# Performance work log

Hardware: AMD Instinct MI355X
Metric: run time of the kernel (lower is better)

The kernel has to match this reference:

```python
import jax, jax.numpy as jnp
import numpy as np

B, S, R, H, NH, HD = 32, 1026, 256, 1024, 16, 64

def setup_inputs() -> dict:
    key = jax.random.key(0)
    ks = jax.random.split(key, 8)
    sc = 0.02
    return {
        "q_low": jax.random.normal(ks[0], (B, S, R), jnp.float32),
        "k_low": jax.random.normal(ks[1], (B, S, R), jnp.float32),
        "v_low": jax.random.normal(ks[2], (B, S, R), jnp.float32),
        "Wq": jax.random.normal(ks[3], (R, H), jnp.float32) * sc,
        "bq": jnp.zeros((H,), jnp.float32),
        "Wk": jax.random.normal(ks[4], (R, H), jnp.float32) * sc,
        "bk": jnp.zeros((H,), jnp.float32),
        "Wv": jax.random.normal(ks[5], (R, H), jnp.float32) * sc,
        "bv": jnp.zeros((H,), jnp.float32),
        "Wo_down": jax.random.normal(ks[6], (H, R), jnp.float32) * sc,
    }

def reference(q_low, k_low, v_low, Wq, bq, Wk, bk, Wv, bv, Wo_down):
    # Up-project low-rank activations to full Q, K, V: [B,S,R] @ [R,H] -> [B,S,H]
    q = q_low @ Wq + bq
    k = k_low @ Wk + bk
    v = v_low @ Wv + bv
    # split heads: [B,S,NH,HD] -> [B,NH,S,HD]
    def split(x):
        return x.reshape(B, S, NH, HD).transpose(0, 2, 1, 3)
    qh, kh, vh = split(q), split(k), split(v)
    scores = jnp.einsum('bhqd,bhkd->bhqk', qh, kh) / jnp.sqrt(jnp.float32(HD))
    probs = jax.nn.softmax(scores, axis=-1)  # dropout p=0
    ctx = jnp.einsum('bhqk,bhkd->bhqd', probs, vh)
    ctx = ctx.transpose(0, 2, 1, 3).reshape(B, S, H)
    # Down-project with low-rank activation (gelu)
    out_low = jax.nn.gelu(ctx @ Wo_down, approximate=False)
    return out_low
```

## Files before the change

### kernel.cpp

```cpp
#include <hip/hip_runtime.h>
#include <hip/hip_bf16.h>
#include <math.h>

using short8   = __attribute__((ext_vector_type(8))) short;
using floatx4  = __attribute__((ext_vector_type(4))) float;
using floatx16 = __attribute__((ext_vector_type(16))) float;

#define B_N  32
#define S_N  1026
#define R_N  256
#define H_N  1024
#define NH_N 16
#define HD_N 64
#define SP_N 1088
#define KTILES 17

__device__ __forceinline__ float bf2f(__hip_bfloat16 x) { return __bfloat162float(x); }
__device__ __forceinline__ __hip_bfloat16 f2bf(float x) { return __float2bfloat16(x); }

__device__ __forceinline__ float fast_exp2(float x) {
#if __has_builtin(__builtin_amdgcn_exp2f)
    return __builtin_amdgcn_exp2f(x);
#else
    return exp2f(x);
#endif
}

__device__ __forceinline__ unsigned cvtpk(float lo, float hi_) {
    unsigned r;
    asm("v_cvt_pk_bf16_f32 %0, %1, %2" : "=v"(r) : "v"(lo), "v"(hi_));
    return r;
}

__device__ __forceinline__ void gl_lds16(const void* g, void* l) {
    __builtin_amdgcn_global_load_lds(
        (const __attribute__((address_space(1))) unsigned int*)g,
        (__attribute__((address_space(3))) unsigned int*)l, 16, 0, 0);
}

__device__ __forceinline__ short8 cvt8(const float* __restrict__ p) {
    floatx4 a = *(const floatx4*)p;
    floatx4 b = *(const floatx4*)(p + 4);
    short8 o;
    __hip_bfloat16* op = (__hip_bfloat16*)&o;
    op[0] = f2bf(a[0]); op[1] = f2bf(a[1]); op[2] = f2bf(a[2]); op[3] = f2bf(a[3]);
    op[4] = f2bf(b[0]); op[5] = f2bf(b[1]); op[6] = f2bf(b[2]); op[7] = f2bf(b[3]);
    return o;
}

__global__ __launch_bounds__(256) void transpose_kernel(const float* __restrict__ in,
                                                        __hip_bfloat16* __restrict__ out,
                                                        int K, int N) {
    __shared__ __hip_bfloat16 t[32][33];
    const int k0 = blockIdx.x * 32, n0 = blockIdx.y * 32;
    const int tx = threadIdx.x & 31, ty = threadIdx.x >> 5;
#pragma unroll
    for (int j = 0; j < 32; j += 8)
        t[ty + j][tx] = f2bf(in[(size_t)(k0 + ty + j) * N + n0 + tx]);
    __syncthreads();
#pragma unroll
    for (int j = 0; j < 32; j += 8)
        out[(size_t)(n0 + ty + j) * K + k0 + tx] = t[tx][ty + j];
}

__global__ __launch_bounds__(256) void cvtx_kernel(
    const float* __restrict__ q, const float* __restrict__ k, const float* __restrict__ v,
    __hip_bfloat16* __restrict__ oq, __hip_bfloat16* __restrict__ ok,
    __hip_bfloat16* __restrict__ ov, int n8) {
    int idx = blockIdx.x * 256 + threadIdx.x;
    if (idx >= n8) return;
    const float* s = (blockIdx.y == 0) ? q : (blockIdx.y == 1) ? k : v;
    __hip_bfloat16* d = (blockIdx.y == 0) ? oq : (blockIdx.y == 1) ? ok : ov;
    *(short8*)(d + (size_t)idx * 8) = cvt8(s + (size_t)idx * 8);
}

__global__ void padv_kernel(__hip_bfloat16* __restrict__ Vt, int total) {
    int idx = blockIdx.x * 256 + threadIdx.x;
    if (idx < total) {
        int p  = idx % (SP_N - S_N);
        int rd = idx / (SP_N - S_N);
        Vt[(size_t)rd * SP_N + S_N + p] = f2bf(0.f);
    }
}

template <int MODE>
__global__ __launch_bounds__(256) void proj_kernel(
    const __hip_bfloat16* __restrict__ X,
    const __hip_bfloat16* __restrict__ WT,
    const float* __restrict__ bias,
    __hip_bfloat16* __restrict__ out, int Mc, float oscale) {
    __shared__ __hip_bfloat16 As[128][32];
    __shared__ __hip_bfloat16 Bs[128][32];
    const int tid  = threadIdx.x;
    const int wave = tid >> 6, lane = tid & 63;
    const int quad = lane >> 4, l16 = lane & 15;
    const int tm = blockIdx.x * 128, tn = blockIdx.y * 128;
    const int mw = (wave >> 1) * 64, nw = (wave & 1) * 64;
    const int lrow = lane >> 2, lchunk = lane & 3;

    floatx4 acc[4][4] = {};

    const int g0 = wave, g1 = wave + 4;
    int ra0 = tm + g0 * 16 + lrow; if (ra0 >= Mc) ra0 = Mc - 1;
    int ra1 = tm + g1 * 16 + lrow; if (ra1 >= Mc) ra1 = Mc - 1;
    const int rb0 = tn + g0 * 16 + lrow, rb1 = tn + g1 * 16 + lrow;

    for (int kk = 0; kk < R_N; kk += 32) {
        __syncthreads();
        gl_lds16(X  + (size_t)ra0 * R_N + kk + lchunk * 8, &As[g0 * 16][0]);
        gl_lds16(X  + (size_t)ra1 * R_N + kk + lchunk * 8, &As[g1 * 16][0]);
        gl_lds16(WT + (size_t)rb0 * R_N + kk + lchunk * 8, &Bs[g0 * 16][0]);
        gl_lds16(WT + (size_t)rb1 * R_N + kk + lchunk * 8, &Bs[g1 * 16][0]);
        __syncthreads();
        short8 af[4], bfr[4];
#pragma unroll
        for (int mb = 0; mb < 4; ++mb) af[mb]  = *(short8*)&As[mw + mb * 16 + l16][quad * 8];
#pragma unroll
        for (int nb = 0; nb < 4; ++nb) bfr[nb] = *(short8*)&Bs[nw + nb * 16 + l16][quad * 8];
#pragma unroll
        for (int mb = 0; mb < 4; ++mb)
#pragma unroll
            for (int nb = 0; nb < 4; ++nb) {
                if (MODE == 0)
                    acc[mb][nb] = __builtin_amdgcn_mfma_f32_16x16x32_bf16(af[mb], bfr[nb], acc[mb][nb], 0, 0, 0);
                else
                    acc[mb][nb] = __builtin_amdgcn_mfma_f32_16x16x32_bf16(bfr[nb], af[mb], acc[mb][nb], 0, 0, 0);
            }
    }

#pragma unroll
    for (int mb = 0; mb < 4; ++mb)
#pragma unroll
        for (int nb = 0; nb < 4; ++nb)
#pragma unroll
            for (int r = 0; r < 4; ++r) {
                int m, n;
                if (MODE == 0) { m = tm + mw + mb * 16 + quad * 4 + r; n = tn + nw + nb * 16 + l16; }
                else           { n = tn + nw + nb * 16 + quad * 4 + r; m = tm + mw + mb * 16 + l16; }
                if (m >= Mc) continue;
                float v = oscale * (acc[mb][nb][r] + bias[n]);
                int bl = m / S_N, s = m - bl * S_N;
                int h = n >> 6, d = n & 63;
                size_t off = (MODE == 0)
                    ? ((size_t)((bl * NH_N + h) * S_N + s)) * HD_N + d
                    : ((size_t)((bl * NH_N + h) * HD_N + d)) * SP_N + s;
                out[off] = f2bf(v);
            }
}

__global__ __launch_bounds__(256, 3) void attn_kernel(
    const __hip_bfloat16* __restrict__ Qh,
    const __hip_bfloat16* __restrict__ Kh,
    const __hip_bfloat16* __restrict__ Vt,
    __hip_bfloat16* __restrict__ ctx) {
    __shared__ __hip_bfloat16 Kl[2][64][64];
    __shared__ __hip_bfloat16 Vl[2][64][64];

    const int bh  = blockIdx.x;
    const int q0  = blockIdx.y * 128;
    const int tid = threadIdx.x;
    const int wave = tid >> 6, lane = tid & 63;
    const int c = lane & 31, hi = lane >> 5, c7 = c & 7;
    const size_t base  = (size_t)bh * S_N * HD_N;
    const size_t vbase = (size_t)bh * HD_N * SP_N;

    const int lr = lane >> 3;
    const int sc = (lane & 7) ^ lr;

    short8 qf[4];
    {
        int qrow = q0 + wave * 32 + c;
        if (qrow > S_N - 1) qrow = S_N - 1;
        const __hip_bfloat16* qp = Qh + base + (size_t)qrow * HD_N + hi * 8;
#pragma unroll
        for (int i = 0; i < 4; ++i) qf[i] = *(const short8*)(qp + 16 * i);
    }

    floatx16 oacc[2] = {};
    float lsum = 0.f;

    auto stage = [&](int bb, int kt) {
#pragma unroll
        for (int j = 0; j < 2; ++j) {
            int r = 16 * wave + 8 * j + lr;
            int krow = kt + r;
            if (krow > S_N - 1) krow = S_N - 1;
            gl_lds16(Kh + base + (size_t)krow * HD_N + sc * 8,
                     &Kl[bb][16 * wave + 8 * j][0]);
            gl_lds16(Vt + vbase + (size_t)r * SP_N + kt + sc * 8,
                     &Vl[bb][16 * wave + 8 * j][0]);
        }
    };

    stage(0, 0);
    __syncthreads();

    int bb = 0;
    for (int t = 0; t < KTILES; ++t) {
        const int kt = t * 64;
        if (t + 1 < KTILES) stage(bb ^ 1, kt + 64);
        const bool last = (kt + 64 > S_N);

        short8 pa[2][2];
#pragma unroll
        for (int sub = 0; sub < 2; ++sub) {
            floatx16 sacc = {};
#pragma unroll
            for (int i = 0; i < 4; ++i) {
                short8 kf = *(const short8*)&Kl[bb][32 * sub + c][(((2 * i + hi) ^ c7) << 3)];
                sacc = __builtin_amdgcn_mfma_f32_32x32x16_bf16(kf, qf[i], sacc, 0, 0, 0);
            }
            float ps[16];
            if (!last) {
#pragma unroll
                for (int r = 0; r < 16; ++r) ps[r] = fast_exp2(sacc[r]);
            } else {
#pragma unroll
                for (int r = 0; r < 16; ++r) {
                    int key = kt + 32 * sub + (r & 3) + 8 * (r >> 2) + 4 * hi;
                    ps[r] = (key < S_N) ? fast_exp2(sacc[r]) : 0.f;
                }
            }
#pragma unroll
            for (int r = 0; r < 16; ++r) lsum += ps[r];
#pragma unroll
            for (int step = 0; step < 2; ++step) {
                unsigned w0 = cvtpk(ps[8 * step + 0], ps[8 * step + 1]);
                unsigned w1 = cvtpk(ps[8 * step + 2], ps[8 * step + 3]);
                unsigned w2 = cvtpk(ps[8 * step + 4], ps[8 * step + 5]);
                unsigned w3 = cvtpk(ps[8 * step + 6], ps[8 * step + 7]);
                asm("v_permlane32_swap_b32 %0, %1" : "+v"(w0), "+v"(w2));
                asm("v_permlane32_swap_b32 %0, %1" : "+v"(w1), "+v"(w3));
                union { unsigned u[4]; short8 s; } fu;
                fu.u[0] = w0; fu.u[1] = w1; fu.u[2] = w2; fu.u[3] = w3;
                pa[sub][step] = fu.s;
            }
        }

#pragma unroll
        for (int db = 0; db < 2; ++db)
#pragma unroll
            for (int sub = 0; sub < 2; ++sub)
#pragma unroll
                for (int step = 0; step < 2; ++step) {
                    short8 vf = *(const short8*)
                        &Vl[bb][32 * db + c][((((sub * 2 + step) * 2 + hi) ^ c7) << 3)];
                    oacc[db] = __builtin_amdgcn_mfma_f32_32x32x16_bf16(pa[sub][step], vf, oacc[db], 0, 0, 0);
                }

        __syncthreads();
        bb ^= 1;
    }

    lsum += __shfl_xor(lsum, 32);
    float rs = 1.0f / lsum;

    const int bl = bh / NH_N, h = bh - bl * NH_N;
    const int srow0 = q0 + wave * 32;
#pragma unroll
    for (int r = 0; r < 16; ++r) {
        int q = (r & 3) + 8 * (r >> 2) + 4 * hi;
        float rr = __shfl(rs, q, 32);
        int s = srow0 + q;
        if (s < S_N) {
            size_t o = ((size_t)(bl * S_N + s)) * H_N + h * HD_N + c;
            ctx[o]      = f2bf(oacc[0][r] * rr);
            ctx[o + 32] = f2bf(oacc[1][r] * rr);
        }
    }
}

__global__ __launch_bounds__(256) void dproj_kernel(
    const __hip_bfloat16* __restrict__ X,
    const __hip_bfloat16* __restrict__ WT,
    float* __restrict__ out,
    int Mc) {
    __shared__ __hip_bfloat16 As[128][32];
    __shared__ __hip_bfloat16 Bs[128][32];
    const int tid  = threadIdx.x;
    const int wave = tid >> 6, lane = tid & 63;
    const int quad = lane >> 4, l16 = lane & 15;
    const int tm = blockIdx.x * 128, tn = blockIdx.y * 128;
    const int mw = (wave >> 1) * 64, nw = (wave & 1) * 64;
    const int lrow = lane >> 2, lchunk = lane & 3;

    floatx4 acc[4][4] = {};

    const int g0 = wave, g1 = wave + 4;
    int ra0 = tm + g0 * 16 + lrow; if (ra0 >= Mc) ra0 = Mc - 1;
    int ra1 = tm + g1 * 16 + lrow; if (ra1 >= Mc) ra1 = Mc - 1;
    const int rb0 = tn + g0 * 16 + lrow, rb1 = tn + g1 * 16 + lrow;

    for (int kk = 0; kk < H_N; kk += 32) {
        __syncthreads();
        gl_lds16(X  + (size_t)ra0 * H_N + kk + lchunk * 8, &As[g0 * 16][0]);
        gl_lds16(X  + (size_t)ra1 * H_N + kk + lchunk * 8, &As[g1 * 16][0]);
        gl_lds16(WT + (size_t)rb0 * H_N + kk + lchunk * 8, &Bs[g0 * 16][0]);
        gl_lds16(WT + (size_t)rb1 * H_N + kk + lchunk * 8, &Bs[g1 * 16][0]);
        __syncthreads();
        short8 af[4], bfr[4];
#pragma unroll
        for (int mb = 0; mb < 4; ++mb) af[mb]  = *(short8*)&As[mw + mb * 16 + l16][quad * 8];
#pragma unroll
        for (int nb = 0; nb < 4; ++nb) bfr[nb] = *(short8*)&Bs[nw + nb * 16 + l16][quad * 8];
#pragma unroll
        for (int mb = 0; mb < 4; ++mb)
#pragma unroll
            for (int nb = 0; nb < 4; ++nb)
                acc[mb][nb] = __builtin_amdgcn_mfma_f32_16x16x32_bf16(af[mb], bfr[nb], acc[mb][nb], 0, 0, 0);
    }

#pragma unroll
    for (int mb = 0; mb < 4; ++mb)
#pragma unroll
        for (int nb = 0; nb < 4; ++nb)
#pragma unroll
            for (int r = 0; r < 4; ++r) {
                int m = tm + mw + mb * 16 + quad * 4 + r;
                int n = tn + nw + nb * 16 + l16;
                if (m >= Mc) continue;
                float x = acc[mb][nb][r];
                float g = 0.5f * x * (1.0f + erff(x * 0.70710678118654752f));
                out[(size_t)m * R_N + n] = g;
            }
}

extern "C" void kernel_launch(void* const* d_in, const int* in_sizes, int n_in,
                              void* d_out, int out_size, void* d_ws, size_t ws_size,
                              hipStream_t stream) {
    const float* q_low = (const float*)d_in[0];
    const float* k_low = (const float*)d_in[1];
    const float* v_low = (const float*)d_in[2];
    const float* Wq    = (const float*)d_in[3];
    const float* bq    = (const float*)d_in[4];
    const float* Wk    = (const float*)d_in[5];
    const float* bk    = (const float*)d_in[6];
    const float* Wv    = (const float*)d_in[7];
    const float* bv    = (const float*)d_in[8];
    const float* Wo    = (const float*)d_in[9];
    float* out = (float*)d_out;
    (void)in_sizes; (void)n_in; (void)out_size;

    const float QSCALE = 0.125f * 1.44269504088896f;
    const size_t SZ_W = (size_t)H_N * R_N * 2;

    int C = 32;
    while (C > 1) {
        size_t qk = (size_t)C * NH_N * S_N * HD_N * 2;
        size_t vv = (size_t)C * NH_N * HD_N * SP_N * 2;
        size_t cx = (size_t)C * S_N * H_N * 2;
        if (4 * SZ_W + 2 * qk + vv + cx <= ws_size) break;
        C >>= 1;
    }

    char* ws = (char*)d_ws;
    const size_t SZ_QK = (size_t)C * NH_N * S_N * HD_N * 2;
    const size_t SZ_V  = (size_t)C * NH_N * HD_N * SP_N * 2;
    __hip_bfloat16* WqT = (__hip_bfloat16*)(ws);
    __hip_bfloat16* WkT = (__hip_bfloat16*)(ws + SZ_W);
    __hip_bfloat16* WvT = (__hip_bfloat16*)(ws + 2 * SZ_W);
    __hip_bfloat16* WoT = (__hip_bfloat16*)(ws + 3 * SZ_W);
    __hip_bfloat16* Qc  = (__hip_bfloat16*)(ws + 4 * SZ_W);
    __hip_bfloat16* Kc  = (__hip_bfloat16*)(ws + 4 * SZ_W + SZ_QK);
    __hip_bfloat16* Vc  = (__hip_bfloat16*)(ws + 4 * SZ_W + 2 * SZ_QK);
    __hip_bfloat16* ctc = (__hip_bfloat16*)(ws + 4 * SZ_W + 2 * SZ_QK + SZ_V);

    {
        dim3 tg(R_N / 32, H_N / 32);
        transpose_kernel<<<tg, 256, 0, stream>>>(Wq, WqT, R_N, H_N);
        transpose_kernel<<<tg, 256, 0, stream>>>(Wk, WkT, R_N, H_N);
        transpose_kernel<<<tg, 256, 0, stream>>>(Wv, WvT, R_N, H_N);
        dim3 to(H_N / 32, R_N / 32);
        transpose_kernel<<<to, 256, 0, stream>>>(Wo, WoT, H_N, R_N);
    }

    {
        int total = C * NH_N * HD_N * (SP_N - S_N);
        padv_kernel<<<(total + 255) / 256, 256, 0, stream>>>(Vc, total);
    }

    for (int c0 = 0; c0 < B_N; c0 += C) {
        const int Mc = C * S_N;
        const size_t xoff = (size_t)c0 * S_N * R_N;

        __hip_bfloat16* Xq = ctc;
        __hip_bfloat16* Xk = ctc + (size_t)Mc * R_N;
        __hip_bfloat16* Xv = ctc + 2 * (size_t)Mc * R_N;
        {
            int n8 = Mc * R_N / 8;
            dim3 cg((n8 + 255) / 256, 3);
            cvtx_kernel<<<cg, 256, 0, stream>>>(q_low + xoff, k_low + xoff, v_low + xoff,
                                                Xq, Xk, Xv, n8);
        }

        dim3 pg((Mc + 127) / 128, H_N / 128);
        proj_kernel<0><<<pg, 256, 0, stream>>>(Xq, WqT, bq, Qc, Mc, QSCALE);
        proj_kernel<0><<<pg, 256, 0, stream>>>(Xk, WkT, bk, Kc, Mc, 1.0f);
        proj_kernel<1><<<pg, 256, 0, stream>>>(Xv, WvT, bv, Vc, Mc, 1.0f);

        dim3 ag(C * NH_N, (S_N + 127) / 128);
        attn_kernel<<<ag, 256, 0, stream>>>(Qc, Kc, Vc, ctc);

        dim3 dg((Mc + 127) / 128, R_N / 128);
        dproj_kernel<<<dg, 256, 0, stream>>>(ctc, WoT, out + xoff, Mc);
    }
}
```

Before: 632.4 us.

## Double-buffer projection GEMMs, merge QKV and weight-transpose launches, add MFMA priority hints

```diff
diff --git a/kernel.cpp b/kernel.cpp
--- a/kernel.cpp
+++ b/kernel.cpp
@@ -46,6 +46,24 @@
     op[0] = f2bf(a[0]); op[1] = f2bf(a[1]); op[2] = f2bf(a[2]); op[3] = f2bf(a[3]);
     op[4] = f2bf(b[0]); op[5] = f2bf(b[1]); op[6] = f2bf(b[2]); op[7] = f2bf(b[3]);
     return o;
+}
+
+__global__ __launch_bounds__(256) void transpose3_kernel(
+    const float* __restrict__ a, const float* __restrict__ b, const float* __restrict__ c,
+    __hip_bfloat16* __restrict__ oa, __hip_bfloat16* __restrict__ ob,
+    __hip_bfloat16* __restrict__ oc, int K, int N) {
+    __shared__ __hip_bfloat16 t[32][33];
+    const float* in = (blockIdx.z == 0) ? a : (blockIdx.z == 1) ? b : c;
+    __hip_bfloat16* out = (blockIdx.z == 0) ? oa : (blockIdx.z == 1) ? ob : oc;
+    const int k0 = blockIdx.x * 32, n0 = blockIdx.y * 32;
+    const int tx = threadIdx.x & 31, ty = threadIdx.x >> 5;
+#pragma unroll
+    for (int j = 0; j < 32; j += 8)
+        t[ty + j][tx] = f2bf(in[(size_t)(k0 + ty + j) * N + n0 + tx]);
+    __syncthreads();
+#pragma unroll
+    for (int j = 0; j < 32; j += 8)
+        out[(size_t)(n0 + ty + j) * K + k0 + tx] = t[tx][ty + j];
 }
 
 __global__ __launch_bounds__(256) void transpose_kernel(const float* __restrict__ in,
@@ -83,14 +101,25 @@
     }
 }
 
-template <int MODE>
-__global__ __launch_bounds__(256) void proj_kernel(
-    const __hip_bfloat16* __restrict__ X,
-    const __hip_bfloat16* __restrict__ WT,
-    const float* __restrict__ bias,
-    __hip_bfloat16* __restrict__ out, int Mc, float oscale) {
-    __shared__ __hip_bfloat16 As[128][32];
-    __shared__ __hip_bfloat16 Bs[128][32];
+__global__ __launch_bounds__(256) void qkvproj_kernel(
+    const __hip_bfloat16* __restrict__ Xq, const __hip_bfloat16* __restrict__ Xk,
+    const __hip_bfloat16* __restrict__ Xv,
+    const __hip_bfloat16* __restrict__ WqT, const __hip_bfloat16* __restrict__ WkT,
+    const __hip_bfloat16* __restrict__ WvT,
+    const float* __restrict__ bq, const float* __restrict__ bk,
+    const float* __restrict__ bv,
+    __hip_bfloat16* __restrict__ Qc, __hip_bfloat16* __restrict__ Kc,
+    __hip_bfloat16* __restrict__ Vc, int Mc, float qscale) {
+    __shared__ __hip_bfloat16 As[2][128][32];
+    __shared__ __hip_bfloat16 Bs[2][128][32];
+    const int z = blockIdx.z;
+    const __hip_bfloat16* X  = (z == 0) ? Xq  : (z == 1) ? Xk  : Xv;
+    const __hip_bfloat16* WT = (z == 0) ? WqT : (z == 1) ? WkT : WvT;
+    const float* bias        = (z == 0) ? bq  : (z == 1) ? bk  : bv;
+    __hip_bfloat16* out      = (z == 0) ? Qc  : (z == 1) ? Kc  : Vc;
+    const float oscale = (z == 0) ? qscale : 1.0f;
+    const int mode = (z == 2);
+
     const int tid  = threadIdx.x;
     const int wave = tid >> 6, lane = tid & 63;
     const int quad = lane >> 4, l16 = lane & 15;
@@ -105,27 +134,38 @@
     int ra1 = tm + g1 * 16 + lrow; if (ra1 >= Mc) ra1 = Mc - 1;
     const int rb0 = tn + g0 * 16 + lrow, rb1 = tn + g1 * 16 + lrow;
 
-    for (int kk = 0; kk < R_N; kk += 32) {
+    auto stage = [&](int bb, int kk) {
+        gl_lds16(X  + (size_t)ra0 * R_N + kk + lchunk * 8, &As[bb][g0 * 16][0]);
+        gl_lds16(X  + (size_t)ra1 * R_N + kk + lchunk * 8, &As[bb][g1 * 16][0]);
+        gl_lds16(WT + (size_t)rb0 * R_N + kk + lchunk * 8, &Bs[bb][g0 * 16][0]);
+        gl_lds16(WT + (size_t)rb1 * R_N + kk + lchunk * 8, &Bs[bb][g1 * 16][0]);
+    };
+
+    stage(0, 0);
+    __syncthreads();
+
+    for (int t = 0; t < R_N / 32; ++t) {
+        const int bb = t & 1;
+        if (t + 1 < R_N / 32) stage(bb ^ 1, (t + 1) * 32);
+        short8 af[4], bfr[4];
+#pragma unroll
+        for (int mb = 0; mb < 4; ++mb) af[mb]  = *(short8*)&As[bb][mw + mb * 16 + l16][quad * 8];
+#pragma unroll
+        for (int nb = 0; nb < 4; ++nb) bfr[nb] = *(short8*)&Bs[bb][nw + nb * 16 + l16][quad * 8];
+        if (mode == 0) {
+#pragma unroll
+            for (int mb = 0; mb < 4; ++mb)
+#pragma unroll
+                for (int nb = 0; nb < 4; ++nb)
+                    acc[mb][nb] = __builtin_amdgcn_mfma_f32_16x16x32_bf16(af[mb], bfr[nb], acc[mb][nb], 0, 0, 0);
+        } else {
+#pragma unroll
+            for (int mb = 0; mb < 4; ++mb)
+#pragma unroll
+                for (int nb = 0; nb < 4; ++nb)
+                    acc[mb][nb] = __builtin_amdgcn_mfma_f32_16x16x32_bf16(bfr[nb], af[mb], acc[mb][nb], 0, 0, 0);
+        }
         __syncthreads();
-        gl_lds16(X  + (size_t)ra0 * R_N + kk + lchunk * 8, &As[g0 * 16][0]);
-        gl_lds16(X  + (size_t)ra1 * R_N + kk + lchunk * 8, &As[g1 * 16][0]);
-        gl_lds16(WT + (size_t)rb0 * R_N + kk + lchunk * 8, &Bs[g0 * 16][0]);
-        gl_lds16(WT + (size_t)rb1 * R_N + kk + lchunk * 8, &Bs[g1 * 16][0]);
-        __syncthreads();
-        short8 af[4], bfr[4];
-#pragma unroll
-        for (int mb = 0; mb < 4; ++mb) af[mb]  = *(short8*)&As[mw + mb * 16 + l16][quad * 8];
-#pragma unroll
-        for (int nb = 0; nb < 4; ++nb) bfr[nb] = *(short8*)&Bs[nw + nb * 16 + l16][quad * 8];
-#pragma unroll
-        for (int mb = 0; mb < 4; ++mb)
-#pragma unroll
-            for (int nb = 0; nb < 4; ++nb) {
-                if (MODE == 0)
-                    acc[mb][nb] = __builtin_amdgcn_mfma_f32_16x16x32_bf16(af[mb], bfr[nb], acc[mb][nb], 0, 0, 0);
-                else
-                    acc[mb][nb] = __builtin_amdgcn_mfma_f32_16x16x32_bf16(bfr[nb], af[mb], acc[mb][nb], 0, 0, 0);
-            }
     }
 
 #pragma unroll
@@ -135,13 +175,13 @@
 #pragma unroll
             for (int r = 0; r < 4; ++r) {
                 int m, n;
-                if (MODE == 0) { m = tm + mw + mb * 16 + quad * 4 + r; n = tn + nw + nb * 16 + l16; }
+                if (mode == 0) { m = tm + mw + mb * 16 + quad * 4 + r; n = tn + nw + nb * 16 + l16; }
                 else           { n = tn + nw + nb * 16 + quad * 4 + r; m = tm + mw + mb * 16 + l16; }
                 if (m >= Mc) continue;
                 float v = oscale * (acc[mb][nb][r] + bias[n]);
                 int bl = m / S_N, s = m - bl * S_N;
                 int h = n >> 6, d = n & 63;
-                size_t off = (MODE == 0)
+                size_t off = (mode == 0)
                     ? ((size_t)((bl * NH_N + h) * S_N + s)) * HD_N + d
                     : ((size_t)((bl * NH_N + h) * HD_N + d)) * SP_N + s;
                 out[off] = f2bf(v);
@@ -205,11 +245,13 @@
 #pragma unroll
         for (int sub = 0; sub < 2; ++sub) {
             floatx16 sacc = {};
+            __builtin_amdgcn_s_setprio(1);
 #pragma unroll
             for (int i = 0; i < 4; ++i) {
                 short8 kf = *(const short8*)&Kl[bb][32 * sub + c][(((2 * i + hi) ^ c7) << 3)];
                 sacc = __builtin_amdgcn_mfma_f32_32x32x16_bf16(kf, qf[i], sacc, 0, 0, 0);
             }
+            __builtin_amdgcn_s_setprio(0);
             float ps[16];
             if (!last) {
 #pragma unroll
@@ -237,6 +279,7 @@
             }
         }
 
+        __builtin_amdgcn_s_setprio(1);
 #pragma unroll
         for (int db = 0; db < 2; ++db)
 #pragma unroll
@@ -247,6 +290,7 @@
                         &Vl[bb][32 * db + c][((((sub * 2 + step) * 2 + hi) ^ c7) << 3)];
                     oacc[db] = __builtin_amdgcn_mfma_f32_32x32x16_bf16(pa[sub][step], vf, oacc[db], 0, 0, 0);
                 }
+        __builtin_amdgcn_s_setprio(0);
 
         __syncthreads();
         bb ^= 1;
@@ -275,8 +319,8 @@
     const __hip_bfloat16* __restrict__ WT,
     float* __restrict__ out,
     int Mc) {
-    __shared__ __hip_bfloat16 As[128][32];
-    __shared__ __hip_bfloat16 Bs[128][32];
+    __shared__ __hip_bfloat16 As[2][128][32];
+    __shared__ __hip_bfloat16 Bs[2][128][32];
     const int tid  = threadIdx.x;
     const int wave = tid >> 6, lane = tid & 63;
     const int quad = lane >> 4, l16 = lane & 15;
@@ -291,23 +335,30 @@
     int ra1 = tm + g1 * 16 + lrow; if (ra1 >= Mc) ra1 = Mc - 1;
     const int rb0 = tn + g0 * 16 + lrow, rb1 = tn + g1 * 16 + lrow;
 
-    for (int kk = 0; kk < H_N; kk += 32) {
-        __syncthreads();
-        gl_lds16(X  + (size_t)ra0 * H_N + kk + lchunk * 8, &As[g0 * 16][0]);
-        gl_lds16(X  + (size_t)ra1 * H_N + kk + lchunk * 8, &As[g1 * 16][0]);
-        gl_lds16(WT + (size_t)rb0 * H_N + kk + lchunk * 8, &Bs[g0 * 16][0]);
-        gl_lds16(WT + (size_t)rb1 * H_N + kk + lchunk * 8, &Bs[g1 * 16][0]);
-        __syncthreads();
+    auto stage = [&](int bb, int kk) {
+        gl_lds16(X  + (size_t)ra0 * H_N + kk + lchunk * 8, &As[bb][g0 * 16][0]);
+        gl_lds16(X  + (size_t)ra1 * H_N + kk + lchunk * 8, &As[bb][g1 * 16][0]);
+        gl_lds16(WT + (size_t)rb0 * H_N + kk + lchunk * 8, &Bs[bb][g0 * 16][0]);
+        gl_lds16(WT + (size_t)rb1 * H_N + kk + lchunk * 8, &Bs[bb][g1 * 16][0]);
+    };
+
+    stage(0, 0);
+    __syncthreads();
+
+    for (int t = 0; t < H_N / 32; ++t) {
+        const int bb = t & 1;
+        if (t + 1 < H_N / 32) stage(bb ^ 1, (t + 1) * 32);
         short8 af[4], bfr[4];
 #pragma unroll
-        for (int mb = 0; mb < 4; ++mb) af[mb]  = *(short8*)&As[mw + mb * 16 + l16][quad * 8];
-#pragma unroll
-        for (int nb = 0; nb < 4; ++nb) bfr[nb] = *(short8*)&Bs[nw + nb * 16 + l16][quad * 8];
+        for (int mb = 0; mb < 4; ++mb) af[mb]  = *(short8*)&As[bb][mw + mb * 16 + l16][quad * 8];
+#pragma unroll
+        for (int nb = 0; nb < 4; ++nb) bfr[nb] = *(short8*)&Bs[bb][nw + nb * 16 + l16][quad * 8];
 #pragma unroll
         for (int mb = 0; mb < 4; ++mb)
 #pragma unroll
             for (int nb = 0; nb < 4; ++nb)
                 acc[mb][nb] = __builtin_amdgcn_mfma_f32_16x16x32_bf16(af[mb], bfr[nb], acc[mb][nb], 0, 0, 0);
+        __syncthreads();
     }
 
 #pragma unroll
@@ -366,10 +417,8 @@
     __hip_bfloat16* ctc = (__hip_bfloat16*)(ws + 4 * SZ_W + 2 * SZ_QK + SZ_V);
 
     {
-        dim3 tg(R_N / 32, H_N / 32);
-        transpose_kernel<<<tg, 256, 0, stream>>>(Wq, WqT, R_N, H_N);
-        transpose_kernel<<<tg, 256, 0, stream>>>(Wk, WkT, R_N, H_N);
-        transpose_kernel<<<tg, 256, 0, stream>>>(Wv, WvT, R_N, H_N);
+        dim3 tg(R_N / 32, H_N / 32, 3);
+        transpose3_kernel<<<tg, 256, 0, stream>>>(Wq, Wk, Wv, WqT, WkT, WvT, R_N, H_N);
         dim3 to(H_N / 32, R_N / 32);
         transpose_kernel<<<to, 256, 0, stream>>>(Wo, WoT, H_N, R_N);
     }
@@ -393,10 +442,9 @@
                                                 Xq, Xk, Xv, n8);
         }
 
-        dim3 pg((Mc + 127) / 128, H_N / 128);
-        proj_kernel<0><<<pg, 256, 0, stream>>>(Xq, WqT, bq, Qc, Mc, QSCALE);
-        proj_kernel<0><<<pg, 256, 0, stream>>>(Xk, WkT, bk, Kc, Mc, 1.0f);
-        proj_kernel<1><<<pg, 256, 0, stream>>>(Xv, WvT, bv, Vc, Mc, 1.0f);
+        dim3 pg((Mc + 127) / 128, H_N / 128, 3);
+        qkvproj_kernel<<<pg, 256, 0, stream>>>(Xq, Xk, Xv, WqT, WkT, WvT,
+                                               bq, bk, bv, Qc, Kc, Vc, Mc, QSCALE);
 
         dim3 ag(C * NH_N, (S_N + 127) / 128);
         attn_kernel<<<ag, 256, 0, stream>>>(Qc, Kc, Vc, ctc);
```

Result: no change. 643.4 us (+1.7%).
